# Kernel tuning notes

Hardware: AMD Instinct MI355X
Metric: run time of the kernel (lower is better)

## Reference

```python
import jax, jax.numpy as jnp
import numpy as np

NV, P, C, H, O = 50000, 32, 4, 64, 128
EPS = 1e-5


def _bn(x, g, b, m, v):
    # inference-mode BatchNorm1d over channel dim
    return (x - m) * jax.lax.rsqrt(v + EPS) * g + b


def setup_inputs() -> dict:
    key = jax.random.key(0)
    ks = jax.random.split(key, 16)
    voxel_features = jax.random.normal(ks[0], (NV, P, C), jnp.float32)
    voxel_num_points = jax.random.randint(ks[1], (NV,), 1, P + 1).astype(jnp.int64)
    def lin(k, fin, fout):
        kw, kb = jax.random.split(k)
        s = 1.0 / np.sqrt(fin)
        W = jax.random.uniform(kw, (fin, fout), jnp.float32, -s, s)
        b = jax.random.uniform(kb, (fout,), jnp.float32, -s, s)
        return W, b
    W1, b1 = lin(ks[2], C, H)
    W2, b2 = lin(ks[3], H, H)
    W3, b3 = lin(ks[4], H, O)
    g1 = jax.random.uniform(ks[5], (H,), jnp.float32, 0.5, 1.5)
    be1 = jax.random.normal(ks[6], (H,), jnp.float32) * 0.1
    m1 = jax.random.normal(ks[7], (H,), jnp.float32) * 0.1
    v1 = jax.random.uniform(ks[8], (H,), jnp.float32, 0.5, 1.5)
    g2 = jax.random.uniform(ks[9], (H,), jnp.float32, 0.5, 1.5)
    be2 = jax.random.normal(ks[10], (H,), jnp.float32) * 0.1
    m2 = jax.random.normal(ks[11], (H,), jnp.float32) * 0.1
    v2 = jax.random.uniform(ks[12], (H,), jnp.float32, 0.5, 1.5)
    return dict(voxel_features=voxel_features, voxel_num_points=voxel_num_points,
                W1=W1, b1=b1, g1=g1, be1=be1, m1=m1, v1=v1,
                W2=W2, b2=b2, g2=g2, be2=be2, m2=m2, v2=v2,
                W3=W3, b3=b3)


def reference(voxel_features, voxel_num_points,
              W1, b1, g1, be1, m1, v1,
              W2, b2, g2, be2, m2, v2,
              W3, b3):
    nv, p, c = voxel_features.shape
    x = voxel_features.reshape(-1, c)                 # (NV*P, C)
    x = jax.nn.relu(_bn(x @ W1 + b1, g1, be1, m1, v1))
    x = jax.nn.relu(_bn(x @ W2 + b2, g2, be2, m2, v2))
    x = x @ W3 + b3                                   # (NV*P, O)
    x = x.reshape(nv, p, -1)
    mask = jnp.arange(p)[None, :] < voxel_num_points[:, None]  # (NV, P)
    # original multiplies by mask then masked-fills -inf; net effect is -inf fill
    x = jnp.where(mask[:, :, None], x, -jnp.inf)
    return jnp.max(x, axis=1)                         # (NV, O)
```

## Files before the change

kernel.cpp:

```cpp
#include <hip/hip_runtime.h>
#include <math.h>

#define NVOX 50000
#define PPTS 32
#define HDIM 64
#define ODIM 128
#define EPSBN 1e-5f

typedef _Float16 f16x8 __attribute__((ext_vector_type(8)));
typedef _Float16 f16x4 __attribute__((ext_vector_type(4)));
typedef float f32x4 __attribute__((ext_vector_type(4)));

#define WS_W1C 0
#define WS_W2T 512
#define WS_W3T 4608
#define WS_F32_BYTE 25600
#define FOLD_THREADS 12992

__device__ __host__ inline int permch(int p) {
    return ((p >> 4) & 1) * 32 + ((p >> 2) & 3) * 8 + ((p >> 5) & 1) * 4 + (p & 3);
}

__global__ void vfe_fold(
    const float* __restrict__ W1, const float* __restrict__ b1,
    const float* __restrict__ g1, const float* __restrict__ be1,
    const float* __restrict__ m1, const float* __restrict__ v1,
    const float* __restrict__ W2, const float* __restrict__ b2,
    const float* __restrict__ g2, const float* __restrict__ be2,
    const float* __restrict__ m2, const float* __restrict__ v2,
    const float* __restrict__ W3, const float* __restrict__ b3,
    _Float16* __restrict__ wsh, float* __restrict__ wsf)
{
    int t = blockIdx.x * 256 + threadIdx.x;
    if (t < 512) {
        int p = t >> 3, i = t & 7;
        int ch = permch(p);
        float s1 = g1[ch] * rsqrtf(v1[ch] + EPSBN);
        float val;
        if (i < 4)      val = W1[i * 64 + ch] * s1;
        else if (i == 4) val = (b1[ch] - m1[ch]) * s1 + be1[ch];
        else             val = 0.f;
        wsh[WS_W1C + t] = (_Float16)val;
    } else if (t < 4608) {
        int e = t - 512;
        int p = e >> 6, ch = e & 63;
        int chp = permch(p);
        float s2 = g2[chp] * rsqrtf(v2[chp] + EPSBN);
        wsh[t] = (_Float16)(W2[ch * 64 + chp] * s2);
    } else if (t < 12800) {
        int e = t - 4608;
        int o = e >> 6, ch = e & 63;
        wsh[t] = (_Float16)W3[ch * 128 + o];
    } else if (t < 12864) {
        int i = t - 12800;
        float s2 = g2[i] * rsqrtf(v2[i] + EPSBN);
        wsf[i] = (b2[i] - m2[i]) * s2 + be2[i];
    } else if (t < FOLD_THREADS) {
        int i = t - 12864;
        wsf[64 + i] = b3[i];
    }
}

__global__ __launch_bounds__(256, 3) void vfe_mfma(
    const float* __restrict__ vf, const int* __restrict__ vnp,
    const _Float16* __restrict__ wsh, const float* __restrict__ wsf,
    float* __restrict__ out)
{
    __shared__ __align__(16) _Float16 sW3[ODIM * HDIM];

    const int tid  = threadIdx.x;
    const int wave = tid >> 6;
    const int lane = tid & 63;
    const int q    = lane >> 4;
    const int m16  = lane & 15;

    const int wavebase = blockIdx.x * 256 + wave * 64;
    const int voxA = wavebase >> 5;

#pragma unroll
    for (int i = 0; i < 4; ++i) {
        int G = tid + 256 * i;
        int o = G >> 3, gl = G & 7;
        int ph = gl ^ (o & 7);
        f16x8 v = *(const f16x8*)&wsh[WS_W3T + o * 64 + gl * 8];
        *(f16x8*)&sW3[o * 64 + ph * 8] = v;
    }

    const int nA = vnp[voxA];
    const int nB = vnp[voxA + 1];

    f16x8 a1[4];
#pragma unroll
    for (int mt = 0; mt < 4; ++mt) {
        f16x8 t = *(const f16x8*)&wsh[WS_W1C + (m16 + 16 * mt) * 8];
        a1[mt] = (q == 0) ? t : (f16x8)0;
    }
    f16x8 a2[4][2];
#pragma unroll
    for (int mt = 0; mt < 4; ++mt)
#pragma unroll
        for (int kk = 0; kk < 2; ++kk)
            a2[mt][kk] = *(const f16x8*)&wsh[WS_W2T + (m16 + 16 * mt) * 64 + kk * 32 + q * 8];
    f32x4 c2v[4];
#pragma unroll
    for (int mt = 0; mt < 4; ++mt)
        c2v[mt] = *(const f32x4*)(wsf + (mt & 1) * 32 + q * 8 + (mt >> 1) * 4);

    float4 xv[4];
#pragma unroll
    for (int g = 0; g < 4; ++g)
        if (q == 0)
            xv[g] = *(const float4*)(vf + ((size_t)wavebase + g * 16 + m16) * 4);

    __syncthreads();

    f16x8 a3[4][2];
#pragma unroll
    for (int g = 0; g < 4; ++g) {
        f16x8 b = (f16x8)0;
        if (q == 0) {
            b[0] = (_Float16)xv[g].x; b[1] = (_Float16)xv[g].y;
            b[2] = (_Float16)xv[g].z; b[3] = (_Float16)xv[g].w;
            b[4] = (_Float16)1.0f;
        }
        f32x4 p1[4];
#pragma unroll
        for (int mt = 0; mt < 4; ++mt) {
            f32x4 z = {0.f, 0.f, 0.f, 0.f};
            p1[mt] = __builtin_amdgcn_mfma_f32_16x16x32_f16(a1[mt], b, z, 0, 0, 0);
        }
        f16x8 b20, b21;
#pragma unroll
        for (int r = 0; r < 4; ++r) {
            b20[r]     = (_Float16)fmaxf(p1[0][r], 0.f);
            b20[4 + r] = (_Float16)fmaxf(p1[2][r], 0.f);
            b21[r]     = (_Float16)fmaxf(p1[1][r], 0.f);
            b21[4 + r] = (_Float16)fmaxf(p1[3][r], 0.f);
        }
        f32x4 p2[4];
#pragma unroll
        for (int mt = 0; mt < 4; ++mt) {
            f32x4 acc = c2v[mt];
            acc = __builtin_amdgcn_mfma_f32_16x16x32_f16(a2[mt][0], b20, acc, 0, 0, 0);
            acc = __builtin_amdgcn_mfma_f32_16x16x32_f16(a2[mt][1], b21, acc, 0, 0, 0);
            p2[mt] = acc;
        }
#pragma unroll
        for (int r = 0; r < 4; ++r) {
            a3[g][0][r]     = (_Float16)fmaxf(p2[0][r], 0.f);
            a3[g][0][4 + r] = (_Float16)fmaxf(p2[2][r], 0.f);
            a3[g][1][r]     = (_Float16)fmaxf(p2[1][r], 0.f);
            a3[g][1][4 + r] = (_Float16)fmaxf(p2[3][r], 0.f);
        }
    }

    f32x4 macc4[4];
#pragma unroll
    for (int g = 0; g < 4; ++g) {
        const int n = (g < 2) ? nA : nB;
        const int slotbase = (g & 1) * 16 + q * 4;
#pragma unroll
        for (int r = 0; r < 4; ++r)
            macc4[g][r] = (slotbase + r < n) ? 0.f : -INFINITY;
    }

    float vmA[8], vmB[8];
#pragma unroll
    for (int nt = 0; nt < 8; ++nt) { vmA[nt] = -INFINITY; vmB[nt] = -INFINITY; }

#pragma unroll
    for (int nt = 0; nt < 8; ++nt) {
        const int o = nt * 16 + m16;
        f16x8 b30 = *(const f16x8*)&sW3[o * 64 + ((q    ) ^ (m16 & 7)) * 8];
        f16x8 b31 = *(const f16x8*)&sW3[o * 64 + ((4 + q) ^ (m16 & 7)) * 8];
#pragma unroll
        for (int g = 0; g < 4; ++g) {
            f32x4 acc = macc4[g];
            acc = __builtin_amdgcn_mfma_f32_16x16x32_f16(a3[g][0], b30, acc, 0, 0, 0);
            acc = __builtin_amdgcn_mfma_f32_16x16x32_f16(a3[g][1], b31, acc, 0, 0, 0);
            float m0 = fmaxf(fmaxf(acc[0], acc[1]), fmaxf(acc[2], acc[3]));
            if (g < 2) vmA[nt] = fmaxf(vmA[nt], m0);
            else       vmB[nt] = fmaxf(vmB[nt], m0);
        }
    }

    float b3r[8];
#pragma unroll
    for (int nt = 0; nt < 8; ++nt) b3r[nt] = wsf[64 + nt * 16 + m16];

#pragma unroll
    for (int nt = 0; nt < 8; ++nt) {
        float t0 = vmA[nt];
        t0 = fmaxf(t0, __shfl_xor(t0, 16));
        t0 = fmaxf(t0, __shfl_xor(t0, 32));
        float t1 = vmB[nt];
        t1 = fmaxf(t1, __shfl_xor(t1, 16));
        t1 = fmaxf(t1, __shfl_xor(t1, 32));
        if (q == 0) out[(size_t)(voxA + 0) * ODIM + nt * 16 + m16] = t0 + b3r[nt];
        if (q == 1) out[(size_t)(voxA + 1) * ODIM + nt * 16 + m16] = t1 + b3r[nt];
    }
}

extern "C" void kernel_launch(void* const* d_in, const int* in_sizes, int n_in,
                              void* d_out, int out_size, void* d_ws, size_t ws_size,
                              hipStream_t stream) {
    const float* vf  = (const float*)d_in[0];
    const int*   vnp = (const int*)d_in[1];
    const float* W1  = (const float*)d_in[2];
    const float* b1  = (const float*)d_in[3];
    const float* g1  = (const float*)d_in[4];
    const float* be1 = (const float*)d_in[5];
    const float* m1  = (const float*)d_in[6];
    const float* v1  = (const float*)d_in[7];
    const float* W2  = (const float*)d_in[8];
    const float* b2  = (const float*)d_in[9];
    const float* g2  = (const float*)d_in[10];
    const float* be2 = (const float*)d_in[11];
    const float* m2  = (const float*)d_in[12];
    const float* v2  = (const float*)d_in[13];
    const float* W3  = (const float*)d_in[14];
    const float* b3  = (const float*)d_in[15];
    float* out = (float*)d_out;

    _Float16* wsh = (_Float16*)d_ws;
    float*    wsf = (float*)((char*)d_ws + WS_F32_BYTE);

    vfe_fold<<<(FOLD_THREADS + 255) / 256, 256, 0, stream>>>(
        W1, b1, g1, be1, m1, v1, W2, b2, g2, be2, m2, v2, W3, b3, wsh, wsf);

    const int blocks = (NVOX * PPTS) / 256;
    vfe_mfma<<<blocks, 256, 0, stream>>>(vf, vnp, wsh, wsf, out);
}
```

Baseline: 161.9 us.

## Make MFMA kernel persistent with grid-stride loop and register prefetch of next tile

Replaces the one-tile-per-block launch (6250 blocks) with 625 blocks that each process 10 tiles in a strided loop. Weight staging into registers and LDS (W1, W2, W3, biases) is paid once per block instead of once per tile, and the next tile's point features and point counts are loaded before the current tile is computed. The cost is more live registers for the prefetch buffers under the same launch bounds, and fewer blocks than CUs times occupancy, which may leave tail imbalance or idle waves.

```diff
diff --git a/kernel.cpp b/kernel.cpp
--- a/kernel.cpp
+++ b/kernel.cpp
@@ -16,6 +16,10 @@
 #define WS_W3T 4608
 #define WS_F32_BYTE 25600
 #define FOLD_THREADS 12992
+
+#define BLOCKS_MFMA 625
+#define ITERS 10
+#define PT_STRIDE (BLOCKS_MFMA * 256)
 
 __device__ __host__ inline int permch(int p) {
     return ((p >> 4) & 1) * 32 + ((p >> 2) & 3) * 8 + ((p >> 5) & 1) * 4 + (p & 3);
@@ -74,9 +78,6 @@
     const int q    = lane >> 4;
     const int m16  = lane & 15;
 
-    const int wavebase = blockIdx.x * 256 + wave * 64;
-    const int voxA = wavebase >> 5;
-
 #pragma unroll
     for (int i = 0; i < 4; ++i) {
         int G = tid + 256 * i;
@@ -86,9 +87,6 @@
         *(f16x8*)&sW3[o * 64 + ph * 8] = v;
     }
 
-    const int nA = vnp[voxA];
-    const int nB = vnp[voxA + 1];
-
     f16x8 a1[4];
 #pragma unroll
     for (int mt = 0; mt < 4; ++mt) {
@@ -105,99 +103,123 @@
 #pragma unroll
     for (int mt = 0; mt < 4; ++mt)
         c2v[mt] = *(const f32x4*)(wsf + (mt & 1) * 32 + q * 8 + (mt >> 1) * 4);
-
+    float b3r[8];
+#pragma unroll
+    for (int nt = 0; nt < 8; ++nt) b3r[nt] = wsf[64 + nt * 16 + m16];
+
+    int pbase = blockIdx.x * 256 + wave * 64;
+    int nA = vnp[pbase >> 5];
+    int nB = vnp[(pbase >> 5) + 1];
     float4 xv[4];
 #pragma unroll
     for (int g = 0; g < 4; ++g)
         if (q == 0)
-            xv[g] = *(const float4*)(vf + ((size_t)wavebase + g * 16 + m16) * 4);
+            xv[g] = *(const float4*)(vf + ((size_t)pbase + g * 16 + m16) * 4);
 
     __syncthreads();
 
-    f16x8 a3[4][2];
-#pragma unroll
-    for (int g = 0; g < 4; ++g) {
-        f16x8 b = (f16x8)0;
-        if (q == 0) {
-            b[0] = (_Float16)xv[g].x; b[1] = (_Float16)xv[g].y;
-            b[2] = (_Float16)xv[g].z; b[3] = (_Float16)xv[g].w;
-            b[4] = (_Float16)1.0f;
-        }
-        f32x4 p1[4];
-#pragma unroll
-        for (int mt = 0; mt < 4; ++mt) {
-            f32x4 z = {0.f, 0.f, 0.f, 0.f};
-            p1[mt] = __builtin_amdgcn_mfma_f32_16x16x32_f16(a1[mt], b, z, 0, 0, 0);
-        }
-        f16x8 b20, b21;
-#pragma unroll
-        for (int r = 0; r < 4; ++r) {
-            b20[r]     = (_Float16)fmaxf(p1[0][r], 0.f);
-            b20[4 + r] = (_Float16)fmaxf(p1[2][r], 0.f);
-            b21[r]     = (_Float16)fmaxf(p1[1][r], 0.f);
-            b21[4 + r] = (_Float16)fmaxf(p1[3][r], 0.f);
-        }
-        f32x4 p2[4];
-#pragma unroll
-        for (int mt = 0; mt < 4; ++mt) {
-            f32x4 acc = c2v[mt];
-            acc = __builtin_amdgcn_mfma_f32_16x16x32_f16(a2[mt][0], b20, acc, 0, 0, 0);
-            acc = __builtin_amdgcn_mfma_f32_16x16x32_f16(a2[mt][1], b21, acc, 0, 0, 0);
-            p2[mt] = acc;
-        }
-#pragma unroll
-        for (int r = 0; r < 4; ++r) {
-            a3[g][0][r]     = (_Float16)fmaxf(p2[0][r], 0.f);
-            a3[g][0][4 + r] = (_Float16)fmaxf(p2[2][r], 0.f);
-            a3[g][1][r]     = (_Float16)fmaxf(p2[1][r], 0.f);
-            a3[g][1][4 + r] = (_Float16)fmaxf(p2[3][r], 0.f);
-        }
-    }
-
-    f32x4 macc4[4];
-#pragma unroll
-    for (int g = 0; g < 4; ++g) {
-        const int n = (g < 2) ? nA : nB;
-        const int slotbase = (g & 1) * 16 + q * 4;
-#pragma unroll
-        for (int r = 0; r < 4; ++r)
-            macc4[g][r] = (slotbase + r < n) ? 0.f : -INFINITY;
-    }
-
-    float vmA[8], vmB[8];
-#pragma unroll
-    for (int nt = 0; nt < 8; ++nt) { vmA[nt] = -INFINITY; vmB[nt] = -INFINITY; }
-
-#pragma unroll
-    for (int nt = 0; nt < 8; ++nt) {
-        const int o = nt * 16 + m16;
-        f16x8 b30 = *(const f16x8*)&sW3[o * 64 + ((q    ) ^ (m16 & 7)) * 8];
-        f16x8 b31 = *(const f16x8*)&sW3[o * 64 + ((4 + q) ^ (m16 & 7)) * 8];
+    for (int it = 0; it < ITERS; ++it) {
+        const int nbase = pbase + PT_STRIDE;
+        int nAn, nBn;
+        float4 xn[4];
+        if (it + 1 < ITERS) {
+            nAn = vnp[nbase >> 5];
+            nBn = vnp[(nbase >> 5) + 1];
+#pragma unroll
+            for (int g = 0; g < 4; ++g)
+                if (q == 0)
+                    xn[g] = *(const float4*)(vf + ((size_t)nbase + g * 16 + m16) * 4);
+        }
+        const int voxA = pbase >> 5;
+
+        f16x8 a3[4][2];
 #pragma unroll
         for (int g = 0; g < 4; ++g) {
-            f32x4 acc = macc4[g];
-            acc = __builtin_amdgcn_mfma_f32_16x16x32_f16(a3[g][0], b30, acc, 0, 0, 0);
-            acc = __builtin_amdgcn_mfma_f32_16x16x32_f16(a3[g][1], b31, acc, 0, 0, 0);
-            float m0 = fmaxf(fmaxf(acc[0], acc[1]), fmaxf(acc[2], acc[3]));
-            if (g < 2) vmA[nt] = fmaxf(vmA[nt], m0);
-            else       vmB[nt] = fmaxf(vmB[nt], m0);
-        }
-    }
-
-    float b3r[8];
-#pragma unroll
-    for (int nt = 0; nt < 8; ++nt) b3r[nt] = wsf[64 + nt * 16 + m16];
-
-#pragma unroll
-    for (int nt = 0; nt < 8; ++nt) {
-        float t0 = vmA[nt];
-        t0 = fmaxf(t0, __shfl_xor(t0, 16));
-        t0 = fmaxf(t0, __shfl_xor(t0, 32));
-        float t1 = vmB[nt];
-        t1 = fmaxf(t1, __shfl_xor(t1, 16));
-        t1 = fmaxf(t1, __shfl_xor(t1, 32));
-        if (q == 0) out[(size_t)(voxA + 0) * ODIM + nt * 16 + m16] = t0 + b3r[nt];
-        if (q == 1) out[(size_t)(voxA + 1) * ODIM + nt * 16 + m16] = t1 + b3r[nt];
+            f16x8 b = (f16x8)0;
+            if (q == 0) {
+                b[0] = (_Float16)xv[g].x; b[1] = (_Float16)xv[g].y;
+                b[2] = (_Float16)xv[g].z; b[3] = (_Float16)xv[g].w;
+                b[4] = (_Float16)1.0f;
+            }
+            f32x4 p1[4];
+#pragma unroll
+            for (int mt = 0; mt < 4; ++mt) {
+                f32x4 z = {0.f, 0.f, 0.f, 0.f};
+                p1[mt] = __builtin_amdgcn_mfma_f32_16x16x32_f16(a1[mt], b, z, 0, 0, 0);
+            }
+            f16x8 b20, b21;
+#pragma unroll
+            for (int r = 0; r < 4; ++r) {
+                b20[r]     = (_Float16)fmaxf(p1[0][r], 0.f);
+                b20[4 + r] = (_Float16)fmaxf(p1[2][r], 0.f);
+                b21[r]     = (_Float16)fmaxf(p1[1][r], 0.f);
+                b21[4 + r] = (_Float16)fmaxf(p1[3][r], 0.f);
+            }
+            f32x4 p2[4];
+#pragma unroll
+            for (int mt = 0; mt < 4; ++mt) {
+                f32x4 acc = c2v[mt];
+                acc = __builtin_amdgcn_mfma_f32_16x16x32_f16(a2[mt][0], b20, acc, 0, 0, 0);
+                acc = __builtin_amdgcn_mfma_f32_16x16x32_f16(a2[mt][1], b21, acc, 0, 0, 0);
+                p2[mt] = acc;
+            }
+#pragma unroll
+            for (int r = 0; r < 4; ++r) {
+                a3[g][0][r]     = (_Float16)fmaxf(p2[0][r], 0.f);
+                a3[g][0][4 + r] = (_Float16)fmaxf(p2[2][r], 0.f);
+                a3[g][1][r]     = (_Float16)fmaxf(p2[1][r], 0.f);
+                a3[g][1][4 + r] = (_Float16)fmaxf(p2[3][r], 0.f);
+            }
+        }
+
+        f32x4 macc4[4];
+#pragma unroll
+        for (int g = 0; g < 4; ++g) {
+            const int n = (g < 2) ? nA : nB;
+            const int slotbase = (g & 1) * 16 + q * 4;
+#pragma unroll
+            for (int r = 0; r < 4; ++r)
+                macc4[g][r] = (slotbase + r < n) ? 0.f : -INFINITY;
+        }
+
+        float vmA[8], vmB[8];
+#pragma unroll
+        for (int nt = 0; nt < 8; ++nt) { vmA[nt] = -INFINITY; vmB[nt] = -INFINITY; }
+
+#pragma unroll
+        for (int nt = 0; nt < 8; ++nt) {
+            const int o = nt * 16 + m16;
+            f16x8 b30 = *(const f16x8*)&sW3[o * 64 + ((q    ) ^ (m16 & 7)) * 8];
+            f16x8 b31 = *(const f16x8*)&sW3[o * 64 + ((4 + q) ^ (m16 & 7)) * 8];
+#pragma unroll
+            for (int g = 0; g < 4; ++g) {
+                f32x4 acc = macc4[g];
+                acc = __builtin_amdgcn_mfma_f32_16x16x32_f16(a3[g][0], b30, acc, 0, 0, 0);
+                acc = __builtin_amdgcn_mfma_f32_16x16x32_f16(a3[g][1], b31, acc, 0, 0, 0);
+                float m0 = fmaxf(fmaxf(acc[0], acc[1]), fmaxf(acc[2], acc[3]));
+                if (g < 2) vmA[nt] = fmaxf(vmA[nt], m0);
+                else       vmB[nt] = fmaxf(vmB[nt], m0);
+            }
+        }
+
+#pragma unroll
+        for (int nt = 0; nt < 8; ++nt) {
+            float t0 = vmA[nt];
+            t0 = fmaxf(t0, __shfl_xor(t0, 16));
+            t0 = fmaxf(t0, __shfl_xor(t0, 32));
+            float t1 = vmB[nt];
+            t1 = fmaxf(t1, __shfl_xor(t1, 16));
+            t1 = fmaxf(t1, __shfl_xor(t1, 32));
+            if (q == 0) out[(size_t)(voxA + 0) * ODIM + nt * 16 + m16] = t0 + b3r[nt];
+            if (q == 1) out[(size_t)(voxA + 1) * ODIM + nt * 16 + m16] = t1 + b3r[nt];
+        }
+
+        if (it + 1 < ITERS) {
+            pbase = nbase;
+            nA = nAn; nB = nBn;
+#pragma unroll
+            for (int g = 0; g < 4; ++g) xv[g] = xn[g];
+        }
     }
 }
 
@@ -228,6 +250,5 @@
     vfe_fold<<<(FOLD_THREADS + 255) / 256, 256, 0, stream>>>(
         W1, b1, g1, be1, m1, v1, W2, b2, g2, be2, m2, v2, W3, b3, wsh, wsf);
 
-    const int blocks = (NVOX * PPTS) / 256;
-    vfe_mfma<<<blocks, 256, 0, stream>>>(vf, vnp, wsh, wsf, out);
-}
+    vfe_mfma<<<BLOCKS_MFMA, 256, 0, stream>>>(vf, vnp, wsh, wsf, out);
+}
```

Result: slower. 515.9 us (+218.6%).

## Process two chunks per block and skip fully masked point groups

Applied to the files above, without the earlier changes.

Each block now handles 512 points (two 256-point chunks) instead of 256, which amortizes the W3 shared-memory staging and weight register loads over twice the work and halves the grid. Input loads for both chunks are issued up front. It also skips the MLP and layer-3 MFMAs for the second 16-point half of a voxel when its point count is 16 or fewer, since those rows would be masked to -inf anyway. The costs are more register pressure, fewer blocks for latency hiding, and wave-uniform branches inside the unrolled MFMA code.

```diff
diff --git a/kernel.cpp b/kernel.cpp
--- a/kernel.cpp
+++ b/kernel.cpp
@@ -16,6 +16,7 @@
 #define WS_W3T 4608
 #define WS_F32_BYTE 25600
 #define FOLD_THREADS 12992
+
 
 __device__ __host__ inline int permch(int p) {
     return ((p >> 4) & 1) * 32 + ((p >> 2) & 3) * 8 + ((p >> 5) & 1) * 4 + (p & 3);
@@ -61,6 +62,93 @@
     }
 }
 
+#define VFE_CHUNK(XV, NA, NB, VOXA)                                           \
+  do {                                                                        \
+    const bool actB1_ = ((NA) > 16);                                          \
+    const bool actB3_ = ((NB) > 16);                                          \
+    f16x8 a3[4][2] = {};                                                      \
+    _Pragma("unroll")                                                         \
+    for (int g = 0; g < 4; ++g) {                                             \
+        if (g == 1 && !actB1_) continue;                                      \
+        if (g == 3 && !actB3_) continue;                                      \
+        f16x8 b = (f16x8)0;                                                   \
+        if (q == 0) {                                                         \
+            b[0] = (_Float16)XV[g].x; b[1] = (_Float16)XV[g].y;               \
+            b[2] = (_Float16)XV[g].z; b[3] = (_Float16)XV[g].w;               \
+            b[4] = (_Float16)1.0f;                                            \
+        }                                                                     \
+        f32x4 p1[4];                                                          \
+        _Pragma("unroll")                                                     \
+        for (int mt = 0; mt < 4; ++mt) {                                      \
+            f32x4 z = {0.f, 0.f, 0.f, 0.f};                                   \
+            p1[mt] = __builtin_amdgcn_mfma_f32_16x16x32_f16(a1[mt], b, z, 0, 0, 0); \
+        }                                                                     \
+        f16x8 b20, b21;                                                       \
+        _Pragma("unroll")                                                     \
+        for (int r = 0; r < 4; ++r) {                                         \
+            b20[r]     = (_Float16)fmaxf(p1[0][r], 0.f);                      \
+            b20[4 + r] = (_Float16)fmaxf(p1[2][r], 0.f);                      \
+            b21[r]     = (_Float16)fmaxf(p1[1][r], 0.f);                      \
+            b21[4 + r] = (_Float16)fmaxf(p1[3][r], 0.f);                      \
+        }                                                                     \
+        f32x4 p2[4];                                                          \
+        _Pragma("unroll")                                                     \
+        for (int mt = 0; mt < 4; ++mt) {                                      \
+            f32x4 acc = c2v[mt];                                              \
+            acc = __builtin_amdgcn_mfma_f32_16x16x32_f16(a2[mt][0], b20, acc, 0, 0, 0); \
+            acc = __builtin_amdgcn_mfma_f32_16x16x32_f16(a2[mt][1], b21, acc, 0, 0, 0); \
+            p2[mt] = acc;                                                     \
+        }                                                                     \
+        _Pragma("unroll")                                                     \
+        for (int r = 0; r < 4; ++r) {                                         \
+            a3[g][0][r]     = (_Float16)fmaxf(p2[0][r], 0.f);                 \
+            a3[g][0][4 + r] = (_Float16)fmaxf(p2[2][r], 0.f);                 \
+            a3[g][1][r]     = (_Float16)fmaxf(p2[1][r], 0.f);                 \
+            a3[g][1][4 + r] = (_Float16)fmaxf(p2[3][r], 0.f);                 \
+        }                                                                     \
+    }                                                                         \
+    f32x4 macc4[4];                                                           \
+    _Pragma("unroll")                                                         \
+    for (int g = 0; g < 4; ++g) {                                             \
+        const int n_ = (g < 2) ? (NA) : (NB);                                 \
+        const int slotbase_ = (g & 1) * 16 + q * 4;                           \
+        _Pragma("unroll")                                                     \
+        for (int r = 0; r < 4; ++r)                                           \
+            macc4[g][r] = (slotbase_ + r < n_) ? 0.f : -INFINITY;             \
+    }                                                                         \
+    float vmA[8], vmB[8];                                                     \
+    _Pragma("unroll")                                                         \
+    for (int nt = 0; nt < 8; ++nt) { vmA[nt] = -INFINITY; vmB[nt] = -INFINITY; } \
+    _Pragma("unroll")                                                         \
+    for (int nt = 0; nt < 8; ++nt) {                                          \
+        const int o_ = nt * 16 + m16;                                         \
+        f16x8 b30 = *(const f16x8*)&sW3[o_ * 64 + ((q    ) ^ (m16 & 7)) * 8]; \
+        f16x8 b31 = *(const f16x8*)&sW3[o_ * 64 + ((4 + q) ^ (m16 & 7)) * 8]; \
+        _Pragma("unroll")                                                     \
+        for (int g = 0; g < 4; ++g) {                                         \
+            if (g == 1 && !actB1_) continue;                                  \
+            if (g == 3 && !actB3_) continue;                                  \
+            f32x4 acc = macc4[g];                                             \
+            acc = __builtin_amdgcn_mfma_f32_16x16x32_f16(a3[g][0], b30, acc, 0, 0, 0); \
+            acc = __builtin_amdgcn_mfma_f32_16x16x32_f16(a3[g][1], b31, acc, 0, 0, 0); \
+            float m0 = fmaxf(fmaxf(acc[0], acc[1]), fmaxf(acc[2], acc[3]));   \
+            if (g < 2) vmA[nt] = fmaxf(vmA[nt], m0);                          \
+            else       vmB[nt] = fmaxf(vmB[nt], m0);                          \
+        }                                                                     \
+    }                                                                         \
+    _Pragma("unroll")                                                         \
+    for (int nt = 0; nt < 8; ++nt) {                                          \
+        float t0 = vmA[nt];                                                   \
+        t0 = fmaxf(t0, __shfl_xor(t0, 16));                                   \
+        t0 = fmaxf(t0, __shfl_xor(t0, 32));                                   \
+        float t1 = vmB[nt];                                                   \
+        t1 = fmaxf(t1, __shfl_xor(t1, 16));                                   \
+        t1 = fmaxf(t1, __shfl_xor(t1, 32));                                   \
+        if (q == 0) out[(size_t)((VOXA) + 0) * ODIM + nt * 16 + m16] = t0 + b3r[nt]; \
+        if (q == 1) out[(size_t)((VOXA) + 1) * ODIM + nt * 16 + m16] = t1 + b3r[nt]; \
+    }                                                                         \
+  } while (0)
+
 __global__ __launch_bounds__(256, 3) void vfe_mfma(
     const float* __restrict__ vf, const int* __restrict__ vnp,
     const _Float16* __restrict__ wsh, const float* __restrict__ wsf,
@@ -74,8 +162,10 @@
     const int q    = lane >> 4;
     const int m16  = lane & 15;
 
-    const int wavebase = blockIdx.x * 256 + wave * 64;
-    const int voxA = wavebase >> 5;
+    const int base0 = blockIdx.x * 512 + wave * 64;
+    const int base1 = base0 + 256;
+    const int voxA0 = base0 >> 5;
+    const int voxA1 = base1 >> 5;
 
 #pragma unroll
     for (int i = 0; i < 4; ++i) {
@@ -86,8 +176,18 @@
         *(f16x8*)&sW3[o * 64 + ph * 8] = v;
     }
 
-    const int nA = vnp[voxA];
-    const int nB = vnp[voxA + 1];
+    const int nA0 = vnp[voxA0];
+    const int nB0 = vnp[voxA0 + 1];
+    const int nA1 = vnp[voxA1];
+    const int nB1 = vnp[voxA1 + 1];
+
+    float4 xv0[4], xv1[4];
+#pragma unroll
+    for (int g = 0; g < 4; ++g)
+        if (q == 0) {
+            xv0[g] = *(const float4*)(vf + ((size_t)base0 + g * 16 + m16) * 4);
+            xv1[g] = *(const float4*)(vf + ((size_t)base1 + g * 16 + m16) * 4);
+        }
 
     f16x8 a1[4];
 #pragma unroll
@@ -105,100 +205,14 @@
 #pragma unroll
     for (int mt = 0; mt < 4; ++mt)
         c2v[mt] = *(const f32x4*)(wsf + (mt & 1) * 32 + q * 8 + (mt >> 1) * 4);
-
-    float4 xv[4];
-#pragma unroll
-    for (int g = 0; g < 4; ++g)
-        if (q == 0)
-            xv[g] = *(const float4*)(vf + ((size_t)wavebase + g * 16 + m16) * 4);
+    float b3r[8];
+#pragma unroll
+    for (int nt = 0; nt < 8; ++nt) b3r[nt] = wsf[64 + nt * 16 + m16];
 
     __syncthreads();
 
-    f16x8 a3[4][2];
-#pragma unroll
-    for (int g = 0; g < 4; ++g) {
-        f16x8 b = (f16x8)0;
-        if (q == 0) {
-            b[0] = (_Float16)xv[g].x; b[1] = (_Float16)xv[g].y;
-            b[2] = (_Float16)xv[g].z; b[3] = (_Float16)xv[g].w;
-            b[4] = (_Float16)1.0f;
-        }
-        f32x4 p1[4];
-#pragma unroll
-        for (int mt = 0; mt < 4; ++mt) {
-            f32x4 z = {0.f, 0.f, 0.f, 0.f};
-            p1[mt] = __builtin_amdgcn_mfma_f32_16x16x32_f16(a1[mt], b, z, 0, 0, 0);
-        }
-        f16x8 b20, b21;
-#pragma unroll
-        for (int r = 0; r < 4; ++r) {
-            b20[r]     = (_Float16)fmaxf(p1[0][r], 0.f);
-            b20[4 + r] = (_Float16)fmaxf(p1[2][r], 0.f);
-            b21[r]     = (_Float16)fmaxf(p1[1][r], 0.f);
-            b21[4 + r] = (_Float16)fmaxf(p1[3][r], 0.f);
-        }
-        f32x4 p2[4];
-#pragma unroll
-        for (int mt = 0; mt < 4; ++mt) {
-            f32x4 acc = c2v[mt];
-            acc = __builtin_amdgcn_mfma_f32_16x16x32_f16(a2[mt][0], b20, acc, 0, 0, 0);
-            acc = __builtin_amdgcn_mfma_f32_16x16x32_f16(a2[mt][1], b21, acc, 0, 0, 0);
-            p2[mt] = acc;
-        }
-#pragma unroll
-        for (int r = 0; r < 4; ++r) {
-            a3[g][0][r]     = (_Float16)fmaxf(p2[0][r], 0.f);
-            a3[g][0][4 + r] = (_Float16)fmaxf(p2[2][r], 0.f);
-            a3[g][1][r]     = (_Float16)fmaxf(p2[1][r], 0.f);
-            a3[g][1][4 + r] = (_Float16)fmaxf(p2[3][r], 0.f);
-        }
-    }
-
-    f32x4 macc4[4];
-#pragma unroll
-    for (int g = 0; g < 4; ++g) {
-        const int n = (g < 2) ? nA : nB;
-        const int slotbase = (g & 1) * 16 + q * 4;
-#pragma unroll
-        for (int r = 0; r < 4; ++r)
-            macc4[g][r] = (slotbase + r < n) ? 0.f : -INFINITY;
-    }
-
-    float vmA[8], vmB[8];
-#pragma unroll
-    for (int nt = 0; nt < 8; ++nt) { vmA[nt] = -INFINITY; vmB[nt] = -INFINITY; }
-
-#pragma unroll
-    for (int nt = 0; nt < 8; ++nt) {
-        const int o = nt * 16 + m16;
-        f16x8 b30 = *(const f16x8*)&sW3[o * 64 + ((q    ) ^ (m16 & 7)) * 8];
-        f16x8 b31 = *(const f16x8*)&sW3[o * 64 + ((4 + q) ^ (m16 & 7)) * 8];
-#pragma unroll
-        for (int g = 0; g < 4; ++g) {
-            f32x4 acc = macc4[g];
-            acc = __builtin_amdgcn_mfma_f32_16x16x32_f16(a3[g][0], b30, acc, 0, 0, 0);
-            acc = __builtin_amdgcn_mfma_f32_16x16x32_f16(a3[g][1], b31, acc, 0, 0, 0);
-            float m0 = fmaxf(fmaxf(acc[0], acc[1]), fmaxf(acc[2], acc[3]));
-            if (g < 2) vmA[nt] = fmaxf(vmA[nt], m0);
-            else       vmB[nt] = fmaxf(vmB[nt], m0);
-        }
-    }
-
-    float b3r[8];
-#pragma unroll
-    for (int nt = 0; nt < 8; ++nt) b3r[nt] = wsf[64 + nt * 16 + m16];
-
-#pragma unroll
-    for (int nt = 0; nt < 8; ++nt) {
-        float t0 = vmA[nt];
-        t0 = fmaxf(t0, __shfl_xor(t0, 16));
-        t0 = fmaxf(t0, __shfl_xor(t0, 32));
-        float t1 = vmB[nt];
-        t1 = fmaxf(t1, __shfl_xor(t1, 16));
-        t1 = fmaxf(t1, __shfl_xor(t1, 32));
-        if (q == 0) out[(size_t)(voxA + 0) * ODIM + nt * 16 + m16] = t0 + b3r[nt];
-        if (q == 1) out[(size_t)(voxA + 1) * ODIM + nt * 16 + m16] = t1 + b3r[nt];
-    }
+    VFE_CHUNK(xv0, nA0, nB0, voxA0);
+    VFE_CHUNK(xv1, nA1, nB1, voxA1);
 }
 
 extern "C" void kernel_launch(void* const* d_in, const int* in_sizes, int n_in,
@@ -228,6 +242,6 @@
     vfe_fold<<<(FOLD_THREADS + 255) / 256, 256, 0, stream>>>(
         W1, b1, g1, be1, m1, v1, W2, b2, g2, be2, m2, v2, W3, b3, wsh, wsf);
 
-    const int blocks = (NVOX * PPTS) / 256;
+    const int blocks = (NVOX * PPTS) / 512;
     vfe_mfma<<<blocks, 256, 0, stream>>>(vf, vnp, wsh, wsf, out);
 }
```

Result: slower. 166.6 us (+2.9%).
